# Kernel optimization log

Measured on AMD Instinct MI355X. Metric: run time of the kernel, lower is better.

Reference implementation:

```python
import jax, jax.numpy as jnp
import numpy as np

B, N, F_IN, F_OUT, D = 8, 2048, 256, 128, 3
ALPHA = 0.2       # leaky relu slope
CUT_OFF = 0.1     # distance gate sharpness
NEG_INF = -9e15


def setup_inputs() -> dict:
    key = jax.random.key(0)
    k1, k2, k3, k4 = jax.random.split(key, 4)
    x = jax.random.normal(k1, (B, N, F_IN), dtype=jnp.float32)
    coord = jax.random.normal(k2, (B, N, D), dtype=jnp.float32)
    # xavier_uniform-style scale (gain=1.414); normal init is fine for a reference
    w_std = 1.414 * np.sqrt(2.0 / (F_IN + F_OUT))
    a_std = 1.414 * np.sqrt(2.0 / (2 * F_OUT + 1))
    W = jax.random.normal(k3, (F_IN, F_OUT), dtype=jnp.float32) * w_std
    a = jax.random.normal(k4, (2 * F_OUT, 1), dtype=jnp.float32) * a_std
    return {"x": x, "coord": coord, "W": W, "a": a}


def reference(x, coord, W, a):
    # h: [B, N, F_OUT]
    h = jnp.matmul(x, W)
    # The original builds a_input=[h_i || h_j] and does a_input @ a.
    # Equivalent: e_ij = leaky_relu(h_i @ a[:F] + h_j @ a[F:]).
    f_src = jnp.matmul(h, a[:F_OUT])   # [B, N, 1]
    f_dst = jnp.matmul(h, a[F_OUT:])   # [B, N, 1]
    e = f_src + jnp.swapaxes(f_dst, 1, 2)            # [B, N, N]
    e = jnp.where(e > 0, e, ALPHA * e)               # leaky relu
    # pairwise squared distances -> exponential gate
    diff = coord[:, :, None, :] - coord[:, None, :, :]   # [B, N, N, D]
    loc = jnp.exp(-CUT_OFF * jnp.sum(diff * diff, axis=-1))  # [B, N, N]
    att_logits = jnp.where(loc > 0.01, e * loc, NEG_INF)
    attention = jax.nn.softmax(att_logits, axis=2)
    # dropout is identity in eval mode
    h_prime = jnp.matmul(attention, h)               # [B, N, F_OUT]
    return jax.nn.elu(h_prime)                       # concat=True path
```

## Files before the change

### kernel.cpp

```cpp
#include <hip/hip_runtime.h>
#include <hip/hip_bf16.h>

#define B_    8
#define N_    2048
#define FIN_  256
#define FOUT_ 128
#define NROWS (B_*N_)

typedef __attribute__((ext_vector_type(8))) short short8;
typedef __attribute__((ext_vector_type(4))) float f32x4;

__device__ __forceinline__ float bf2f(unsigned short u) {
  return __uint_as_float(((unsigned int)u) << 16);
}
__device__ __forceinline__ unsigned short f2bf(float f) {
  unsigned int u = __float_as_uint(f);
  u += 0x7FFFu + ((u >> 16) & 1u);
  return (unsigned short)(u >> 16);
}
__device__ __forceinline__ float ldin(const void* p, size_t idx, int isbf) {
  if (isbf) return bf2f(((const unsigned short*)p)[idx]);
  return ((const float*)p)[idx];
}
__device__ __forceinline__ unsigned pk2bf(float a, float b) {
  return (unsigned)f2bf(a) | ((unsigned)f2bf(b) << 16);
}
__device__ __forceinline__ unsigned encf(float f) {
  unsigned u = __float_as_uint(f);
  return (u & 0x80000000u) ? ~u : (u | 0x80000000u);
}
__device__ __forceinline__ float decf(unsigned k) {
  return (k & 0x80000000u) ? __uint_as_float(k ^ 0x80000000u) : __uint_as_float(~k);
}
__device__ __forceinline__ int detect_bf(const void* x, int* cnt) {
  const unsigned short* u = (const unsigned short*)x;
  int c = 0;
  for (int i = threadIdx.x; i < 8192; i += 256) {
    unsigned short v = u[i];
    int e = (v >> 7) & 0xFF;
    if ((e >= 110 && e <= 145) || (v & 0x7FFF) == 0) c++;
  }
  cnt[threadIdx.x] = c;
  __syncthreads();
  for (int s = 128; s > 0; s >>= 1) {
    if (threadIdx.x < s) cnt[threadIdx.x] += cnt[threadIdx.x + s];
    __syncthreads();
  }
  return cnt[0] > 7373;
}

__global__ __launch_bounds__(256)
void k_prep(const void* __restrict__ x, const void* __restrict__ W,
            const void* __restrict__ a,
            unsigned short* __restrict__ WT, float* __restrict__ wa,
            int* __restrict__ flag, unsigned* __restrict__ MdstE) {
  __shared__ int cnt[256];
  const int isbf = detect_bf(x, cnt);
  if (blockIdx.x < 128) {
    int f = blockIdx.x, k = threadIdx.x;
    WT[f * 256 + k] = f2bf(ldin(W, (size_t)k * 128 + f, isbf));
  } else {
    __shared__ float as_s[256];
    int k = threadIdx.x;
    as_s[k] = ldin(a, k, isbf);
    __syncthreads();
    float s = 0.f, d = 0.f;
    for (int f = 0; f < 128; f++) {
      float w = ldin(W, (size_t)k * 128 + f, isbf);
      s += w * as_s[f];
      d += w * as_s[128 + f];
    }
    wa[k] = s;
    wa[256 + k] = d;
    if (k == 0) *flag = isbf;
    if (k < 8) MdstE[k * 32] = 0u;
  }
}

__global__ __launch_bounds__(256)
void k_h(const void* __restrict__ x, const unsigned short* __restrict__ WT,
         const float* __restrict__ wa, const int* __restrict__ flag,
         unsigned short* __restrict__ hT, float* __restrict__ fsrc,
         float* __restrict__ fdst, unsigned* __restrict__ MdstE) {
  __shared__ __align__(16) unsigned short xs[32][264];
  __shared__ float wa_s[512];
  __shared__ float mxs[8];
  const int isbf = *flag;
  const int t    = threadIdx.x;
  const int row0 = blockIdx.x * 32;

  wa_s[t] = wa[t];
  wa_s[256 + t] = wa[256 + t];
  __syncthreads();

  const int c = t & 31;
  float sp[4], dp[4];
  if (isbf) {
    const unsigned short* xu = (const unsigned short*)x;
#pragma unroll
    for (int u = 0; u < 4; u++) {
      int r = u * 8 + (t >> 5);
      short8 sh = *(const short8*)&xu[(size_t)(row0 + r) * FIN_ + c * 8];
      *(short8*)&xs[r][c * 8] = sh;
      float s = 0.f, d = 0.f;
#pragma unroll
      for (int e = 0; e < 8; e++) {
        float xv = bf2f((unsigned short)sh[e]);
        s += xv * wa_s[c * 8 + e];
        d += xv * wa_s[256 + c * 8 + e];
      }
      sp[u] = s; dp[u] = d;
    }
  } else {
    const float* xf = (const float*)x;
#pragma unroll
    for (int u = 0; u < 4; u++) {
      int r = u * 8 + (t >> 5);
      float4 v0 = *(const float4*)&xf[(size_t)(row0 + r) * FIN_ + c * 8];
      float4 v1 = *(const float4*)&xf[(size_t)(row0 + r) * FIN_ + c * 8 + 4];
      float vv[8] = {v0.x, v0.y, v0.z, v0.w, v1.x, v1.y, v1.z, v1.w};
      short8 sh;
      float s = 0.f, d = 0.f;
#pragma unroll
      for (int e = 0; e < 8; e++) {
        sh[e] = (short)f2bf(vv[e]);
        s += vv[e] * wa_s[c * 8 + e];
        d += vv[e] * wa_s[256 + c * 8 + e];
      }
      *(short8*)&xs[r][c * 8] = sh;
      sp[u] = s; dp[u] = d;
    }
  }
#pragma unroll
  for (int off = 16; off >= 1; off >>= 1) {
#pragma unroll
    for (int u = 0; u < 4; u++) {
      sp[u] += __shfl_xor(sp[u], off, 64);
      dp[u] += __shfl_xor(dp[u], off, 64);
    }
  }
  if (c == 0) {
    float lm = -1e30f;
#pragma unroll
    for (int u = 0; u < 4; u++) {
      int r = u * 8 + (t >> 5);
      fsrc[row0 + r] = sp[u];
      fdst[row0 + r] = dp[u];
      lm = fmaxf(lm, dp[u]);
    }
    mxs[t >> 5] = lm;
  }
  __syncthreads();
  if (t == 0) {
    float m8 = mxs[0];
#pragma unroll
    for (int i = 1; i < 8; i++) m8 = fmaxf(m8, mxs[i]);
    atomicMax(&MdstE[(row0 >> 11) * 32], encf(m8));
  }

  const int lane = t & 63, w = t >> 6;
  const int m = lane & 15, quad = lane >> 4;
  const int slab = w >> 1, fh = w & 1;

  f32x4 acc[4];
#pragma unroll
  for (int i = 0; i < 4; i++) acc[i] = (f32x4){0.f, 0.f, 0.f, 0.f};

#pragma unroll
  for (int ks = 0; ks < 8; ks++) {
    short8 ah = *(const short8*)&xs[slab * 16 + m][ks * 32 + quad * 8];
#pragma unroll
    for (int ft = 0; ft < 4; ft++) {
      int f = fh * 64 + ft * 16 + m;
      short8 bh = *(const short8*)&WT[(size_t)f * 256 + ks * 32 + quad * 8];
      acc[ft] = __builtin_amdgcn_mfma_f32_16x16x32_bf16(ah, bh, acc[ft], 0, 0, 0);
    }
  }

  size_t n0 = (size_t)blockIdx.x * 2 + slab;
  unsigned short* hblk = hT + n0 * (FOUT_ * 16);
#pragma unroll
  for (int ft = 0; ft < 4; ft++) {
    int f = fh * 64 + ft * 16 + m;
    *(uint2*)&hblk[f * 16 + quad * 4] = make_uint2(
        pk2bf(acc[ft][0], acc[ft][1]), pk2bf(acc[ft][2], acc[ft][3]));
  }
}

__global__ __launch_bounds__(256, 4)
void k_attn(const unsigned short* __restrict__ hT, const void* __restrict__ coord,
            const float* __restrict__ fsrc, const float* __restrict__ fdst,
            const unsigned* __restrict__ MdstE, const int* __restrict__ flag,
            void* __restrict__ out) {
  const int isbf = *flag;
  const int tid = threadIdx.x;
  const int b   = blockIdx.x >> 7;
  const int q0  = (blockIdx.x & 127) * 16;

  __shared__ __align__(16) float4 cjs[1024];
  __shared__ __align__(16) unsigned short phi[2][16][136];

  const int qA   = tid & 15;
  const int jseg = tid >> 4;
  const size_t qglb = (size_t)b * N_ + q0 + qA;
  const float cq0 = ldin(coord, qglb * 3 + 0, isbf);
  const float cq1 = ldin(coord, qglb * 3 + 1, isbf);
  const float cq2 = ldin(coord, qglb * 3 + 2, isbf);
  const float fsq = fsrc[qglb];
  const float Bq  = fmaxf(0.f, fsq + decf(MdstE[b * 32]));

  const int lane = tid & 63, w = tid >> 6;
  const int m = lane & 15, quad = lane >> 4;
  f32x4 acc[2], accD;
  acc[0] = (f32x4){0.f, 0.f, 0.f, 0.f};
  acc[1] = (f32x4){0.f, 0.f, 0.f, 0.f};
  accD   = (f32x4){0.f, 0.f, 0.f, 0.f};
  const short8 bones = {(short)0x3F80, (short)0x3F80, (short)0x3F80, (short)0x3F80,
                        (short)0x3F80, (short)0x3F80, (short)0x3F80, (short)0x3F80};

  const unsigned short* hTb = hT + (size_t)b * (N_ * FOUT_);
  const int colA = (w * 2 + 0) * 16 + m;
  const int colB = (w * 2 + 1) * 16 + m;
  const int co   = (quad & 1) * 8;
  const int chq  = quad >> 1;

  for (int r = tid; r < 1024; r += 256) {
    size_t jg = (size_t)b * N_ + r;
    cjs[r] = make_float4(ldin(coord, jg * 3 + 0, isbf), ldin(coord, jg * 3 + 1, isbf),
                         ldin(coord, jg * 3 + 2, isbf), fdst[jg]);
  }
  short8 bcur[8], bnxt[8];
#pragma unroll
  for (int ks = 0; ks < 4; ks++) {
    size_t base = (size_t)(ks * 2 + chq) * (FOUT_ * 16) + co;
    bcur[ks * 2 + 0] = *(const short8*)&hTb[base + colA * 16];
    bcur[ks * 2 + 1] = *(const short8*)&hTb[base + colB * 16];
  }
  __syncthreads();

  for (int t = 0; t < 16; t++) {
    if (t == 8) {
      for (int r = tid; r < 1024; r += 256) {
        size_t jg = (size_t)b * N_ + 1024 + r;
        cjs[r] = make_float4(ldin(coord, jg * 3 + 0, isbf), ldin(coord, jg * 3 + 1, isbf),
                             ldin(coord, jg * 3 + 2, isbf), fdst[jg]);
      }
      __syncthreads();
    }
    const int buf = t & 1;

    if (t < 15) {
      const int jcb = (t + 1) * 8;
#pragma unroll
      for (int ks = 0; ks < 4; ks++) {
        size_t base = (size_t)(jcb + ks * 2 + chq) * (FOUT_ * 16) + co;
        bnxt[ks * 2 + 0] = *(const short8*)&hTb[base + colA * 16];
        bnxt[ks * 2 + 1] = *(const short8*)&hTb[base + colB * 16];
      }
    }

    const int jbase = (t & 7) * 128 + jseg * 8;
    unsigned pk[4];
#pragma unroll
    for (int jp = 0; jp < 4; jp++) {
      float pv[2];
#pragma unroll
      for (int h = 0; h < 2; h++) {
        float4 cj = cjs[jbase + jp * 2 + h];
        float dx = cq0 - cj.x, dy = cq1 - cj.y, dz = cq2 - cj.z;
        float d2 = dx * dx + dy * dy + dz * dz;
        float loc = __expf(-0.1f * d2);
        float e = fsq + cj.w;
        e = fmaxf(e, 0.2f * e);
        float p = (d2 < 46.0517f) ? __expf(fmaf(e, loc, -Bq)) : 0.f;
        pv[h] = p;
      }
      pk[jp] = pk2bf(pv[0], pv[1]);
    }
    *(uint4*)&phi[buf][qA][jseg * 8] = make_uint4(pk[0], pk[1], pk[2], pk[3]);
    __syncthreads();

#pragma unroll
    for (int ks = 0; ks < 4; ks++) {
      short8 ah = *(const short8*)&phi[buf][m][ks * 32 + quad * 8];
      acc[0] = __builtin_amdgcn_mfma_f32_16x16x32_bf16(ah, bcur[ks * 2 + 0], acc[0], 0, 0, 0);
      acc[1] = __builtin_amdgcn_mfma_f32_16x16x32_bf16(ah, bcur[ks * 2 + 1], acc[1], 0, 0, 0);
      accD   = __builtin_amdgcn_mfma_f32_16x16x32_bf16(ah, bones, accD, 0, 0, 0);
    }
#pragma unroll
    for (int i = 0; i < 8; i++) bcur[i] = bnxt[i];
  }

#pragma unroll
  for (int f2 = 0; f2 < 2; f2++) {
    int f = (w * 2 + f2) * 16 + m;
#pragma unroll
    for (int r = 0; r < 4; r++) {
      int q = quad * 4 + r;
      float v = acc[f2][r] / fmaxf(accD[r], 1e-30f);
      v = (v > 0.f) ? v : (__expf(v) - 1.0f);
      size_t oidx = ((size_t)(b * N_ + q0 + q)) * FOUT_ + f;
      if (isbf) ((unsigned short*)out)[oidx] = f2bf(v);
      else      ((float*)out)[oidx] = v;
    }
  }
}

extern "C" void kernel_launch(void* const* d_in, const int* in_sizes, int n_in,
                              void* d_out, int out_size, void* d_ws, size_t ws_size,
                              hipStream_t stream) {
  const void* x     = d_in[0];
  const void* coord = d_in[1];
  const void* W     = d_in[2];
  const void* a     = d_in[3];

  int*            flag  = (int*)d_ws;
  unsigned*       MdstE = (unsigned*)d_ws + 64;
  unsigned short* hT    = (unsigned short*)((float*)d_ws + 512);
  unsigned short* WT    = hT + (size_t)NROWS * FOUT_;
  float*          wa    = (float*)(WT + 128 * 256);
  float*          fsrc  = wa + 512;
  float*          fdst  = fsrc + NROWS;

  k_prep<<<129, 256, 0, stream>>>(x, W, a, WT, wa, flag, MdstE);
  k_h   <<<NROWS / 32, 256, 0, stream>>>(x, WT, wa, flag, hT, fsrc, fdst, MdstE);
  k_attn<<<B_ * (N_ / 16), 256, 0, stream>>>(hT, coord, fsrc, fdst, MdstE, flag, d_out);
}
```

Baseline: 139.1 us.

## Pack coords with fdst in k_h and stream per-tile coord chunks in attention

k_h now writes a packed float4 (x,y,z, log2e-scaled fdst) per node, so k_attn loads one aligned float4 instead of three scattered coord loads plus fdst. k_attn replaces its 1024-entry shared coord staging, which reloaded at t==8, with a double-buffered 128-entry tile prefetched into registers one iteration ahead. The exponentials are rewritten in base 2 using the hardware exp2, and bf16 packing uses v_cvt_pk_bf16_f32. The phi column layout changes to strided 32-bit stores and extra workspace is used for cpack. The bf16 rounding now comes from the hardware instruction instead of the manual routine.

```diff
diff --git a/kernel.cpp b/kernel.cpp
--- a/kernel.cpp
+++ b/kernel.cpp
@@ -24,6 +24,13 @@
 }
 __device__ __forceinline__ unsigned pk2bf(float a, float b) {
   return (unsigned)f2bf(a) | ((unsigned)f2bf(b) << 16);
+}
+__device__ __forceinline__ float ex2(float x) {
+#if __has_builtin(__builtin_amdgcn_exp2f)
+  return __builtin_amdgcn_exp2f(x);
+#else
+  return __expf(x * 0.69314718056f);
+#endif
 }
 __device__ __forceinline__ unsigned encf(float f) {
   unsigned u = __float_as_uint(f);
@@ -78,10 +85,11 @@
 }
 
 __global__ __launch_bounds__(256)
-void k_h(const void* __restrict__ x, const unsigned short* __restrict__ WT,
+void k_h(const void* __restrict__ x, const void* __restrict__ coord,
+         const unsigned short* __restrict__ WT,
          const float* __restrict__ wa, const int* __restrict__ flag,
          unsigned short* __restrict__ hT, float* __restrict__ fsrc,
-         float* __restrict__ fdst, unsigned* __restrict__ MdstE) {
+         float4* __restrict__ cpack, unsigned* __restrict__ MdstE) {
   __shared__ __align__(16) unsigned short xs[32][264];
   __shared__ float wa_s[512];
   __shared__ float mxs[8];
@@ -144,8 +152,12 @@
 #pragma unroll
     for (int u = 0; u < 4; u++) {
       int r = u * 8 + (t >> 5);
-      fsrc[row0 + r] = sp[u];
-      fdst[row0 + r] = dp[u];
+      size_t rg = (size_t)(row0 + r);
+      fsrc[rg] = sp[u];
+      cpack[rg] = make_float4(ldin(coord, rg * 3 + 0, isbf),
+                              ldin(coord, rg * 3 + 1, isbf),
+                              ldin(coord, rg * 3 + 2, isbf),
+                              dp[u] * 1.44269504f);
       lm = fmaxf(lm, dp[u]);
     }
     mxs[t >> 5] = lm;
@@ -188,26 +200,24 @@
 }
 
 __global__ __launch_bounds__(256, 4)
-void k_attn(const unsigned short* __restrict__ hT, const void* __restrict__ coord,
-            const float* __restrict__ fsrc, const float* __restrict__ fdst,
-            const unsigned* __restrict__ MdstE, const int* __restrict__ flag,
-            void* __restrict__ out) {
+void k_attn(const unsigned short* __restrict__ hT, const float4* __restrict__ cpack,
+            const float* __restrict__ fsrc, const unsigned* __restrict__ MdstE,
+            const int* __restrict__ flag, void* __restrict__ out) {
   const int isbf = *flag;
   const int tid = threadIdx.x;
   const int b   = blockIdx.x >> 7;
   const int q0  = (blockIdx.x & 127) * 16;
 
-  __shared__ __align__(16) float4 cjs[1024];
+  __shared__ __align__(16) float4 cjs[2][128];
   __shared__ __align__(16) unsigned short phi[2][16][136];
 
   const int qA   = tid & 15;
   const int jseg = tid >> 4;
   const size_t qglb = (size_t)b * N_ + q0 + qA;
-  const float cq0 = ldin(coord, qglb * 3 + 0, isbf);
-  const float cq1 = ldin(coord, qglb * 3 + 1, isbf);
-  const float cq2 = ldin(coord, qglb * 3 + 2, isbf);
-  const float fsq = fsrc[qglb];
-  const float Bq  = fmaxf(0.f, fsq + decf(MdstE[b * 32]));
+  const float4 cq  = cpack[qglb];
+  const float  fsq = fsrc[qglb];
+  const float  fsqL = fsq * 1.44269504f;
+  const float  mBqL = -fmaxf(0.f, fsq + decf(MdstE[b * 32])) * 1.44269504f;
 
   const int lane = tid & 63, w = tid >> 6;
   const int m = lane & 15, quad = lane >> 4;
@@ -219,16 +229,13 @@
                         (short)0x3F80, (short)0x3F80, (short)0x3F80, (short)0x3F80};
 
   const unsigned short* hTb = hT + (size_t)b * (N_ * FOUT_);
+  const float4* cpb = cpack + (size_t)b * N_;
   const int colA = (w * 2 + 0) * 16 + m;
   const int colB = (w * 2 + 1) * 16 + m;
   const int co   = (quad & 1) * 8;
   const int chq  = quad >> 1;
 
-  for (int r = tid; r < 1024; r += 256) {
-    size_t jg = (size_t)b * N_ + r;
-    cjs[r] = make_float4(ldin(coord, jg * 3 + 0, isbf), ldin(coord, jg * 3 + 1, isbf),
-                         ldin(coord, jg * 3 + 2, isbf), fdst[jg]);
-  }
+  if (tid < 128) cjs[0][tid] = cpb[tid];
   short8 bcur[8], bnxt[8];
 #pragma unroll
   for (int ks = 0; ks < 4; ks++) {
@@ -239,14 +246,6 @@
   __syncthreads();
 
   for (int t = 0; t < 16; t++) {
-    if (t == 8) {
-      for (int r = tid; r < 1024; r += 256) {
-        size_t jg = (size_t)b * N_ + 1024 + r;
-        cjs[r] = make_float4(ldin(coord, jg * 3 + 0, isbf), ldin(coord, jg * 3 + 1, isbf),
-                             ldin(coord, jg * 3 + 2, isbf), fdst[jg]);
-      }
-      __syncthreads();
-    }
     const int buf = t & 1;
 
     if (t < 15) {
@@ -258,26 +257,36 @@
         bnxt[ks * 2 + 1] = *(const short8*)&hTb[base + colB * 16];
       }
     }
-
-    const int jbase = (t & 7) * 128 + jseg * 8;
-    unsigned pk[4];
+    float4 cg;
+    if (t < 15 && tid < 128) cg = cpb[(t + 1) * 128 + tid];
+
+    unsigned pks[4];
 #pragma unroll
     for (int jp = 0; jp < 4; jp++) {
-      float pv[2];
-#pragma unroll
-      for (int h = 0; h < 2; h++) {
-        float4 cj = cjs[jbase + jp * 2 + h];
-        float dx = cq0 - cj.x, dy = cq1 - cj.y, dz = cq2 - cj.z;
-        float d2 = dx * dx + dy * dy + dz * dz;
-        float loc = __expf(-0.1f * d2);
-        float e = fsq + cj.w;
-        e = fmaxf(e, 0.2f * e);
-        float p = (d2 < 46.0517f) ? __expf(fmaf(e, loc, -Bq)) : 0.f;
-        pv[h] = p;
-      }
-      pk[jp] = pk2bf(pv[0], pv[1]);
-    }
-    *(uint4*)&phi[buf][qA][jseg * 8] = make_uint4(pk[0], pk[1], pk[2], pk[3]);
+      const float4 cj0 = cjs[buf][2 * jseg + 32 * jp + 0];
+      const float4 cj1 = cjs[buf][2 * jseg + 32 * jp + 1];
+      float dx0 = cq.x - cj0.x, dy0 = cq.y - cj0.y, dz0 = cq.z - cj0.z;
+      float dx1 = cq.x - cj1.x, dy1 = cq.y - cj1.y, dz1 = cq.z - cj1.z;
+      float d20 = fmaf(dz0, dz0, fmaf(dy0, dy0, dx0 * dx0));
+      float d21 = fmaf(dz1, dz1, fmaf(dy1, dy1, dx1 * dx1));
+      float loc0 = ex2(-0.14426950408f * d20);
+      float loc1 = ex2(-0.14426950408f * d21);
+      float xL0 = fsqL + cj0.w, xL1 = fsqL + cj1.w;
+      float eL0 = fmaxf(xL0, 0.2f * xL0);
+      float eL1 = fmaxf(xL1, 0.2f * xL1);
+      float p0 = ex2(fmaf(eL0, loc0, mBqL));
+      float p1 = ex2(fmaf(eL1, loc1, mBqL));
+      p0 = (d20 < 46.0517f) ? p0 : 0.f;
+      p1 = (d21 < 46.0517f) ? p1 : 0.f;
+      unsigned r;
+      asm("v_cvt_pk_bf16_f32 %0, %1, %2" : "=v"(r) : "v"(p0), "v"(p1));
+      pks[jp] = r;
+    }
+#pragma unroll
+    for (int jp = 0; jp < 4; jp++)
+      *(unsigned*)&phi[buf][qA][2 * jseg + 32 * jp] = pks[jp];
+
+    if (t < 15 && tid < 128) cjs[buf ^ 1][tid] = cg;
     __syncthreads();
 
 #pragma unroll
@@ -320,9 +329,9 @@
   unsigned short* WT    = hT + (size_t)NROWS * FOUT_;
   float*          wa    = (float*)(WT + 128 * 256);
   float*          fsrc  = wa + 512;
-  float*          fdst  = fsrc + NROWS;
+  float4*         cpack = (float4*)(fsrc + NROWS);
 
   k_prep<<<129, 256, 0, stream>>>(x, W, a, WT, wa, flag, MdstE);
-  k_h   <<<NROWS / 32, 256, 0, stream>>>(x, WT, wa, flag, hT, fsrc, fdst, MdstE);
-  k_attn<<<B_ * (N_ / 16), 256, 0, stream>>>(hT, coord, fsrc, fdst, MdstE, flag, d_out);
-}
+  k_h   <<<NROWS / 32, 256, 0, stream>>>(x, coord, WT, wa, flag, hT, fsrc, cpack, MdstE);
+  k_attn<<<B_ * (N_ / 16), 256, 0, stream>>>(hT, cpack, fsrc, MdstE, flag, d_out);
+}
```

Result: no change. 139.2 us (+0.1%).
